# Kernel tuning notes

Measured on AMD Instinct MI355X. Metric: run time of the kernel, lower is better.

Reference implementation:

```python
import jax, jax.numpy as jnp
import numpy as np

N_USER, N_BADGE, E = 200_000, 50_000, 5_000_000
NEG_SLOPE = 0.2


def _gat(x_src, x_dst, src, dst, Ws, Wd, a_s, a_d, b, n_dst):
    """Bipartite single-head PyG GATConv (add_self_loops=False)."""
    hs = x_src @ Ws                      # [Ns, C]
    hd = x_dst @ Wd                      # [Nd, C]
    alpha_s = hs @ a_s                   # [Ns]
    alpha_d = hd @ a_d                   # [Nd]
    e = jax.nn.leaky_relu(alpha_s[src] + alpha_d[dst], NEG_SLOPE)  # [E]
    m = jax.ops.segment_max(e, dst, num_segments=n_dst)            # per-dst max
    w = jnp.exp(e - m[dst])
    s = jax.ops.segment_sum(w, dst, num_segments=n_dst) + 1e-16
    alpha = w / s[dst]                   # softmax over incoming edges
    out = jax.ops.segment_sum(alpha[:, None] * hs[src], dst, num_segments=n_dst)
    return out + b


def setup_inputs() -> dict:
    key = jax.random.key(0)
    ks = jax.random.split(key, 40)
    i = [0]
    def nk():
        k = ks[i[0]]; i[0] += 1; return k
    def nrm(shape, scale):
        return jax.random.normal(nk(), shape, jnp.float32) * scale
    inp = {
        "x_user": nrm((N_USER, 64), 1.0),
        "x_badge": nrm((N_BADGE, 64), 1.0),
        "ub_src": jax.random.randint(nk(), (E,), 0, N_USER, jnp.int32),
        "ub_dst": jax.random.randint(nk(), (E,), 0, N_BADGE, jnp.int32),
        "bu_src": jax.random.randint(nk(), (E,), 0, N_BADGE, jnp.int32),
        "bu_dst": jax.random.randint(nk(), (E,), 0, N_USER, jnp.int32),
        "ew_ub": jax.random.uniform(nk(), (E,), jnp.float32),
        "ew_bu": jax.random.uniform(nk(), (E,), jnp.float32),
    }
    s64, s16 = 1.0 / 8.0, 1.0 / 4.0  # ~glorot-ish scales for fan_in 64 / 16
    for rel in ("ub", "bu"):
        inp[f"W1_{rel}_s"] = nrm((64, 16), s64)
        inp[f"W1_{rel}_d"] = nrm((64, 16), s64)
        inp[f"a1_{rel}_s"] = nrm((16,), s16)
        inp[f"a1_{rel}_d"] = nrm((16,), s16)
        inp[f"b1_{rel}"] = jnp.zeros((16,), jnp.float32)
        inp[f"W2_{rel}_s"] = nrm((16, 2), s16)
        inp[f"W2_{rel}_d"] = nrm((16, 2), s16)
        inp[f"a2_{rel}_s"] = nrm((2,), 0.5)
        inp[f"a2_{rel}_d"] = nrm((2,), 0.5)
        inp[f"b2_{rel}"] = jnp.zeros((2,), jnp.float32)
    return inp


def reference(x_user, x_badge, ub_src, ub_dst, bu_src, bu_dst, ew_ub, ew_bu,
              W1_ub_s, W1_ub_d, a1_ub_s, a1_ub_d, b1_ub,
              W1_bu_s, W1_bu_d, a1_bu_s, a1_bu_d, b1_bu,
              W2_ub_s, W2_ub_d, a2_ub_s, a2_ub_d, b2_ub,
              W2_bu_s, W2_bu_d, a2_bu_s, a2_bu_d, b2_bu):
    # layer 1 (edge weights ignored: GATConv has edge_dim=None -> lin_edge is None)
    hb = _gat(x_user, x_badge, ub_src, ub_dst, W1_ub_s, W1_ub_d, a1_ub_s, a1_ub_d, b1_ub, N_BADGE)
    hu = _gat(x_badge, x_user, bu_src, bu_dst, W1_bu_s, W1_bu_d, a1_bu_s, a1_bu_d, b1_bu, N_USER)
    hu = jax.nn.relu(hu)
    hb = jax.nn.relu(hb)
    # layer 2
    ob = _gat(hu, hb, ub_src, ub_dst, W2_ub_s, W2_ub_d, a2_ub_s, a2_ub_d, b2_ub, N_BADGE)
    ou = _gat(hb, hu, bu_src, bu_dst, W2_bu_s, W2_bu_d, a2_bu_s, a2_bu_d, b2_bu, N_USER)
    return (ou, ob)
```

## Files before the change

### kernel.cpp

```cpp
#include <hip/hip_runtime.h>
#include <hip/hip_fp16.h>
#include <math.h>


#define NEG_SLOPE 0.2f
#define PART_PER 4880
#define NBC 196
#define CAPC 27072
#define NHALF 392
#define CAPH 13824
#define SHARD_DIV 50000

__device__ __forceinline__ float lrelu(float x) { return x > 0.f ? x : NEG_SLOPE * x; }

__global__ void k_stageA(
    const int* __restrict__ src0, const int* __restrict__ dst0,
    const int* __restrict__ src1, const int* __restrict__ dst1,
    int nE, int pblocks, unsigned* __restrict__ part0, unsigned* __restrict__ part1,
    int* __restrict__ bcnt,
    const float* __restrict__ xu, const float* __restrict__ xb,
    const float* __restrict__ Wub_s, const float* __restrict__ aub_s,
    const float* __restrict__ Wbu_d, const float* __restrict__ abu_d,
    const float* __restrict__ Wbu_s, const float* __restrict__ abu_s,
    const float* __restrict__ Wub_d, const float* __restrict__ aub_d,
    __half* __restrict__ hs_u, float* __restrict__ as_u, float* __restrict__ ad_u,
    __half* __restrict__ hs_b, float* __restrict__ as_b, float* __restrict__ ad_b,
    int NU, int NB, int gNU, int partBlocks, int nodeBlocks) {
  union Sm {
    struct { unsigned s_sorted[PART_PER]; int h[257]; int ps[256]; int resb[256]; int cur[256]; } p;
    struct { float sW[64 * 16]; float sa[16]; float sv[64]; } n;
  };
  __shared__ Sm sm;
  int t = threadIdx.x;
  int b = blockIdx.x;
  int k = min(nodeBlocks, partBlocks / 2);
  int inter = 3 * k;
  int partIdx = -1, nodeIdx = -1;
  if (b < inter) {
    if ((b % 3) == 2) nodeIdx = b / 3;
    else partIdx = (b / 3) * 2 + (b % 3);
  } else {
    int rem = b - inter;
    int ptail = partBlocks - 2 * k;
    if (rem < ptail) partIdx = 2 * k + rem;
    else nodeIdx = k + (rem - ptail);
  }
  if (partIdx >= 0) {
    int gb = partIdx;
    const int* src; const int* dst; unsigned* part; int* bc; int shift; int mask;
    if (gb < pblocks) { src = src0; dst = dst0; part = part0; bc = bcnt; shift = 8; mask = 255; }
    else { gb -= pblocks; src = src1; dst = dst1; part = part1; bc = bcnt + 256; shift = 10; mask = 1023; }
    int per = (nE + pblocks - 1) / pblocks;
    int beg = gb * per;
    int end = min(beg + per, nE);
    int cnt = end - beg;
    int cnt4 = cnt & ~3;
    sm.p.h[t] = 0;
    __syncthreads();
    for (int i = beg + t * 4; i + 3 < end; i += 1024) {
      int4 d4 = *(const int4*)(dst + i);
      atomicAdd(&sm.p.h[d4.x >> shift], 1);
      atomicAdd(&sm.p.h[d4.y >> shift], 1);
      atomicAdd(&sm.p.h[d4.z >> shift], 1);
      atomicAdd(&sm.p.h[d4.w >> shift], 1);
    }
    for (int i = beg + cnt4 + t; i < end; i += 256) atomicAdd(&sm.p.h[dst[i] >> shift], 1);
    __syncthreads();
    int v = sm.p.h[t];
    sm.p.ps[t] = v;
    __syncthreads();
    for (int off = 1; off < 256; off <<= 1) {
      int u = (t >= off) ? sm.p.ps[t - off] : 0;
      __syncthreads();
      sm.p.ps[t] += u;
      __syncthreads();
    }
    int excl = sm.p.ps[t] - v;
    sm.p.resb[t] = (t < NBC && v > 0) ? atomicAdd(&bc[t], v) : 0;
    __syncthreads();
    sm.p.h[t] = excl;
    sm.p.cur[t] = excl;
    if (t == 255) sm.p.h[256] = excl + v;
    __syncthreads();
    for (int i = beg + t * 4; i + 3 < end; i += 1024) {
      int4 d4 = *(const int4*)(dst + i);
      int4 s4 = *(const int4*)(src + i);
      int r;
      r = atomicAdd(&sm.p.cur[d4.x >> shift], 1);
      sm.p.s_sorted[r] = ((unsigned)(d4.x & mask) << 18) | (unsigned)s4.x;
      r = atomicAdd(&sm.p.cur[d4.y >> shift], 1);
      sm.p.s_sorted[r] = ((unsigned)(d4.y & mask) << 18) | (unsigned)s4.y;
      r = atomicAdd(&sm.p.cur[d4.z >> shift], 1);
      sm.p.s_sorted[r] = ((unsigned)(d4.z & mask) << 18) | (unsigned)s4.z;
      r = atomicAdd(&sm.p.cur[d4.w >> shift], 1);
      sm.p.s_sorted[r] = ((unsigned)(d4.w & mask) << 18) | (unsigned)s4.w;
    }
    for (int i = beg + cnt4 + t; i < end; i += 256) {
      int d = dst[i];
      int r = atomicAdd(&sm.p.cur[d >> shift], 1);
      sm.p.s_sorted[r] = ((unsigned)(d & mask) << 18) | (unsigned)src[i];
    }
    __syncthreads();
    for (int i = t; i < cnt; i += 1024) {
      int i1 = i + 256, i2 = i + 512, i3 = i + 768;
      int lo0 = 0, lo1 = 0, lo2 = 0, lo3 = 0;
      int hi0 = 256, hi1 = 256, hi2 = 256, hi3 = 256;
#pragma unroll
      for (int s = 0; s < 8; ++s) {
        int m0 = (lo0 + hi0) >> 1; if (sm.p.h[m0] <= i)  lo0 = m0; else hi0 = m0;
        int m1 = (lo1 + hi1) >> 1; if (sm.p.h[m1] <= i1) lo1 = m1; else hi1 = m1;
        int m2 = (lo2 + hi2) >> 1; if (sm.p.h[m2] <= i2) lo2 = m2; else hi2 = m2;
        int m3 = (lo3 + hi3) >> 1; if (sm.p.h[m3] <= i3) lo3 = m3; else hi3 = m3;
      }
      { int p = sm.p.resb[lo0] + (i - sm.p.h[lo0]);
        if (p < CAPC) part[(size_t)lo0 * CAPC + p] = sm.p.s_sorted[i]; }
      if (i1 < cnt) { int p = sm.p.resb[lo1] + (i1 - sm.p.h[lo1]);
        if (p < CAPC) part[(size_t)lo1 * CAPC + p] = sm.p.s_sorted[i1]; }
      if (i2 < cnt) { int p = sm.p.resb[lo2] + (i2 - sm.p.h[lo2]);
        if (p < CAPC) part[(size_t)lo2 * CAPC + p] = sm.p.s_sorted[i2]; }
      if (i3 < cnt) { int p = sm.p.resb[lo3] + (i3 - sm.p.h[lo3]);
        if (p < CAPC) part[(size_t)lo3 * CAPC + p] = sm.p.s_sorted[i3]; }
    }
    return;
  }
  int blk = nodeIdx;
  bool us = blk < gNU;
  const float* x  = us ? xu : xb;
  const float* Ws = us ? Wub_s : Wbu_s;
  const float* As = us ? aub_s : abu_s;
  const float* Wd = us ? Wbu_d : Wub_d;
  const float* Ad = us ? abu_d : aub_d;
  __half* hs = us ? hs_u : hs_b;
  float* als = us ? as_u : as_b;
  float* ald = us ? ad_u : ad_b;
  int N = us ? NU : NB;
  for (int i = t; i < 64 * 16; i += 256) sm.n.sW[i] = Ws[i];
  if (t < 16) sm.n.sa[t] = As[t];
  if (t < 64) {
    float s = 0.f;
    for (int c = 0; c < 16; ++c) s += Wd[t * 16 + c] * Ad[c];
    sm.n.sv[t] = s;
  }
  __syncthreads();
  int n = (us ? blk : blk - gNU) * 256 + t;
  if (n >= N) return;
  float acc[16];
#pragma unroll
  for (int c = 0; c < 16; ++c) acc[c] = 0.f;
  float ad = 0.f;
  const float4* xr4 = (const float4*)(x + (size_t)n * 64);
#pragma unroll 4
  for (int f4 = 0; f4 < 16; ++f4) {
    float4 xv4 = xr4[f4];
    float xv[4] = {xv4.x, xv4.y, xv4.z, xv4.w};
#pragma unroll
    for (int q = 0; q < 4; ++q) {
      int f = f4 * 4 + q;
#pragma unroll
      for (int c = 0; c < 16; ++c) acc[c] += xv[q] * sm.n.sW[f * 16 + c];
      ad += xv[q] * sm.n.sv[f];
    }
  }
  float al = 0.f;
#pragma unroll
  for (int c = 0; c < 16; ++c) {
    hs[(size_t)n * 16 + c] = __float2half(acc[c]);
    al += acc[c] * sm.n.sa[c];
  }
  als[n] = al;
  ald[n] = ad;
}

__global__ void k_sort2_both(const unsigned* __restrict__ part0,
                             const unsigned* __restrict__ part1,
                             const int* __restrict__ bcnt,
                             int* __restrict__ col0, int* __restrict__ col1,
                             int* __restrict__ rp0, int* __restrict__ rp1) {
  __shared__ unsigned s_sorted[CAPH];
  __shared__ int hist[512];
  __shared__ int ps[512];
  __shared__ int cur[512];
  __shared__ int s_tot;
  int bb = blockIdx.x;
  const unsigned* part; const int* bc; int* col; int* rp;
  int hsh, hmask, ns, sdiv;
  if (bb < NHALF) { part = part0; bc = bcnt; col = col0; rp = rp0;
                    hsh = 7; hmask = 127; ns = 4; sdiv = SHARD_DIV; }
  else { bb -= NHALF; part = part1; bc = bcnt + 256; col = col1; rp = rp1;
         hsh = 9; hmask = 511; ns = 1; sdiv = 1 << 30; }
  int t = threadIdx.x;
  int f = bb >> 1;
  int half = bb & 1;
  int cnt = min(bc[f], CAPC);
  int cnt4 = cnt & ~3;
  int slot = bb * CAPH;
  const unsigned* pp = part + (size_t)f * CAPC;
  hist[t] = 0;
  __syncthreads();
  for (int i = t * 4; i + 3 < cnt; i += 2048) {
    uint4 e4 = *(const uint4*)(pp + i);
    unsigned ee[4] = {e4.x, e4.y, e4.z, e4.w};
#pragma unroll
    for (int q = 0; q < 4; ++q) {
      int dl = (int)(ee[q] >> 18);
      if ((dl >> hsh) == half) {
        int sv = (int)(ee[q] & 0x3FFFFu);
        int bin = (ns == 4) ? ((dl & hmask) << 2) + sv / sdiv : (dl & hmask);
        atomicAdd(&hist[bin], 1);
      }
    }
  }
  for (int i = cnt4 + t; i < cnt; i += 512) {
    unsigned e = pp[i];
    int dl = (int)(e >> 18);
    if ((dl >> hsh) == half) {
      int sv = (int)(e & 0x3FFFFu);
      int bin = (ns == 4) ? ((dl & hmask) << 2) + sv / sdiv : (dl & hmask);
      atomicAdd(&hist[bin], 1);
    }
  }
  __syncthreads();
  int v = hist[t];
  ps[t] = v;
  __syncthreads();
  for (int off = 1; off < 512; off <<= 1) {
    int u = (t >= off) ? ps[t - off] : 0;
    __syncthreads();
    ps[t] += u;
    __syncthreads();
  }
  int excl = ps[t] - v;
  rp[bb * 513 + t] = slot + excl;
  if (t == 511) {
    int tot = min(ps[511], CAPH);
    rp[bb * 513 + 512] = slot + tot;
    s_tot = tot;
  }
  cur[t] = excl;
  __syncthreads();
  for (int i = t * 4; i + 3 < cnt; i += 2048) {
    uint4 e4 = *(const uint4*)(pp + i);
    unsigned ee[4] = {e4.x, e4.y, e4.z, e4.w};
#pragma unroll
    for (int q = 0; q < 4; ++q) {
      int dl = (int)(ee[q] >> 18);
      if ((dl >> hsh) == half) {
        int sv = (int)(ee[q] & 0x3FFFFu);
        int bin = (ns == 4) ? ((dl & hmask) << 2) + sv / sdiv : (dl & hmask);
        int r = atomicAdd(&cur[bin], 1);
        if (r < CAPH) s_sorted[r] = (unsigned)sv;
      }
    }
  }
  for (int i = cnt4 + t; i < cnt; i += 512) {
    unsigned e = pp[i];
    int dl = (int)(e >> 18);
    if ((dl >> hsh) == half) {
      int sv = (int)(e & 0x3FFFFu);
      int bin = (ns == 4) ? ((dl & hmask) << 2) + sv / sdiv : (dl & hmask);
      int r = atomicAdd(&cur[bin], 1);
      if (r < CAPH) s_sorted[r] = (unsigned)sv;
    }
  }
  __syncthreads();
  int tot = s_tot;
  for (int i = t; i < tot; i += 512) col[slot + i] = (int)s_sorted[i];
}

__device__ __forceinline__ void gat_pipe4(
    const int* __restrict__ col, const float* __restrict__ as,
    const __half* __restrict__ hs, int beg, int end, int j, float adv,
    float (&acc)[16], float& se) {
  int k0 = beg + j;
  if (k0 >= end) return;
  int sv0 = col[k0];
  int k1 = k0 + 4;
  int sv1 = (k1 < end) ? col[k1] : -1;
  float e0 = as[sv0];
  const uint4* hv0 = (const uint4*)(hs + (size_t)sv0 * 16);
  uint4 lo0 = hv0[0], hi0 = hv0[1];
  for (;;) {
    float e1 = 0.f;
    uint4 lo1 = lo0, hi1 = hi0;
    int sv2 = -1;
    int k2 = k1 + 4;
    if (sv1 >= 0) {
      e1 = as[sv1];
      const uint4* hv1 = (const uint4*)(hs + (size_t)sv1 * 16);
      lo1 = hv1[0];
      hi1 = hv1[1];
      sv2 = (k2 < end) ? col[k2] : -1;
    }
    float w = __expf(lrelu(e0 + adv));
    se += w;
    union { uint4 v[2]; __half h[16]; } b;
    b.v[0] = lo0;
    b.v[1] = hi0;
#pragma unroll
    for (int c = 0; c < 16; ++c) acc[c] += w * __half2float(b.h[c]);
    if (sv1 < 0) break;
    e0 = e1;
    lo0 = lo1;
    hi0 = hi1;
    sv1 = sv2;
    k1 = k2;
  }
}

__global__ void k_megaL1(
    const int* __restrict__ rp_ub, const int* __restrict__ col_ub,
    const float* __restrict__ as_u, const float* __restrict__ ad_b,
    const __half* __restrict__ hs_u,
    float* __restrict__ acc_sl, float* __restrict__ se_sl,
    const int* __restrict__ rp_bu, const int* __restrict__ col_bu,
    const float* __restrict__ as_b, const float* __restrict__ ad_u,
    const __half* __restrict__ hs_b,
    const float* __restrict__ b1bu,
    const float* __restrict__ W2ub_s, const float* __restrict__ a2ub_s,
    const float* __restrict__ W2bu_d, const float* __restrict__ a2bu_d,
    float4* __restrict__ pk_u, int NB, int NU, int ubBlocks) {
  __shared__ float sW2[32], sa2[2], sv2[16], sb1[16];
  int t = threadIdx.x;
  if (t < 32) sW2[t] = W2ub_s[t];
  if (t < 2) sa2[t] = a2ub_s[t];
  if (t < 16) {
    float s = 0.f;
    for (int cc = 0; cc < 2; ++cc) s += W2bu_d[t * 2 + cc] * a2bu_d[cc];
    sv2[t] = s;
    sb1[t] = b1bu[t];
  }
  __syncthreads();
  int b = blockIdx.x;
  int j = t & 3;
  if (b < ubBlocks) {
    int xcd = b & 7;
    int s = xcd >> 1;
    int sub = ((b >> 3) << 1) | (xcd & 1);
    int n = sub * 64 + (t >> 2);
    if (n >= NB) return;
    int base = (n >> 7) * 513 + (n & 127) * 4 + s;
    int beg = rp_ub[base], end = rp_ub[base + 1];
    float adv = ad_b[n];
    float acc[16];
#pragma unroll
    for (int c = 0; c < 16; ++c) acc[c] = 0.f;
    float se = 0.f;
    gat_pipe4(col_ub, as_u, hs_u, beg, end, j, adv, acc, se);
#pragma unroll
    for (int m = 1; m < 4; m <<= 1) {
      se += __shfl_xor(se, m, 4);
#pragma unroll
      for (int c = 0; c < 16; ++c) acc[c] += __shfl_xor(acc[c], m, 4);
    }
    if (j == 0) {
      float* o = acc_sl + ((size_t)s * NB + n) * 16;
#pragma unroll
      for (int c = 0; c < 16; ++c) o[c] = acc[c];
      se_sl[s * NB + n] = se;
    }
  } else {
    int n = (b - ubBlocks) * 64 + (t >> 2);
    if (n >= NU) return;
    int base = (n >> 9) * 513 + (n & 511);
    int beg = rp_bu[base], end = rp_bu[base + 1];
    float adv = ad_u[n];
    float acc[16];
#pragma unroll
    for (int c = 0; c < 16; ++c) acc[c] = 0.f;
    float se = 0.f;
    gat_pipe4(col_bu, as_b, hs_b, beg, end, j, adv, acc, se);
#pragma unroll
    for (int m = 1; m < 4; m <<= 1) {
      se += __shfl_xor(se, m, 4);
#pragma unroll
      for (int c = 0; c < 16; ++c) acc[c] += __shfl_xor(acc[c], m, 4);
    }
    if (j == 0) {
      float inv = 1.f / (se + 1e-16f);
      float h0 = 0.f, h1 = 0.f, advn = 0.f;
#pragma unroll
      for (int c = 0; c < 16; ++c) {
        float xv = fmaxf(acc[c] * inv + sb1[c], 0.f);
        h0 += xv * sW2[c * 2];
        h1 += xv * sW2[c * 2 + 1];
        advn += xv * sv2[c];
      }
      pk_u[n] = make_float4(h0 * sa2[0] + h1 * sa2[1], h0, h1, advn);
    }
  }
}

__global__ void k_finL1b(
    const float* __restrict__ acc_sl, const float* __restrict__ se_sl,
    const float* __restrict__ b1ub,
    const float* __restrict__ W2bu_s, const float* __restrict__ a2bu_s,
    const float* __restrict__ W2ub_d, const float* __restrict__ a2ub_d,
    float4* __restrict__ pk_b, int NB) {
  __shared__ float sW2[32], sa2[2], sv2[16], sb1[16];
  int t = threadIdx.x;
  if (t < 32) sW2[t] = W2bu_s[t];
  if (t < 2) sa2[t] = a2bu_s[t];
  if (t < 16) {
    float s = 0.f;
    for (int cc = 0; cc < 2; ++cc) s += W2ub_d[t * 2 + cc] * a2ub_d[cc];
    sv2[t] = s;
    sb1[t] = b1ub[t];
  }
  __syncthreads();
  int n = blockIdx.x * 256 + t;
  if (n >= NB) return;
  float a[16];
#pragma unroll
  for (int c = 0; c < 16; ++c) a[c] = 0.f;
  float se = 0.f;
  for (int s = 0; s < 4; ++s) {
    const float4* p = (const float4*)(acc_sl + ((size_t)s * NB + n) * 16);
    float4 v0 = p[0], v1 = p[1], v2 = p[2], v3 = p[3];
    a[0] += v0.x; a[1] += v0.y; a[2] += v0.z; a[3] += v0.w;
    a[4] += v1.x; a[5] += v1.y; a[6] += v1.z; a[7] += v1.w;
    a[8] += v2.x; a[9] += v2.y; a[10] += v2.z; a[11] += v2.w;
    a[12] += v3.x; a[13] += v3.y; a[14] += v3.z; a[15] += v3.w;
    se += se_sl[s * NB + n];
  }
  float inv = 1.f / (se + 1e-16f);
  float h0 = 0.f, h1 = 0.f, advn = 0.f;
#pragma unroll
  for (int c = 0; c < 16; ++c) {
    float xv = fmaxf(a[c] * inv + sb1[c], 0.f);
    h0 += xv * sW2[c * 2];
    h1 += xv * sW2[c * 2 + 1];
    advn += xv * sv2[c];
  }
  pk_b[n] = make_float4(h0 * sa2[0] + h1 * sa2[1], h0, h1, advn);
}

__global__ void k_gatherL2(
    const int* __restrict__ rp0, const int* __restrict__ col0,
    const int* __restrict__ rp1, const int* __restrict__ col1,
    const float4* __restrict__ pk_u, const float4* __restrict__ pk_b,
    const float* __restrict__ b2ub, const float* __restrict__ b2bu,
    float* __restrict__ ob, float* __restrict__ ou,
    int NB, int NU, int g0) {
  int blk = blockIdx.x;
  const int *rp, *col; const float4 *pksrc, *pkown; const float* bb; float* out;
  int N, lsh, nsg;
  if (blk < g0) { rp = rp0; col = col0; pksrc = pk_u; pkown = pk_b; bb = b2ub;
                  out = ob; N = NB; lsh = 7; nsg = 4; }
  else { blk -= g0; rp = rp1; col = col1; pksrc = pk_b; pkown = pk_u; bb = b2bu;
         out = ou; N = NU; lsh = 9; nsg = 1; }
  int n = blk * 64 + (threadIdx.x >> 2);
  int j = threadIdx.x & 3;
  if (n >= N) return;
  int base = (n >> lsh) * 513 + (n & ((1 << lsh) - 1)) * nsg;
  int beg = rp[base], end = rp[base + nsg];
  float adv = pkown[n].w;
  float a0 = 0.f, a1 = 0.f, se = 0.f;
  int k0 = beg + j;
  if (k0 < end) {
    int c0 = col[k0];
    int k1 = k0 + 4;
    int c1 = (k1 < end) ? col[k1] : -1;
    float4 p0 = pksrc[c0];
    for (;;) {
      float4 p1 = p0;
      int c2 = -1;
      int k2 = k1 + 4;
      if (c1 >= 0) {
        p1 = pksrc[c1];
        c2 = (k2 < end) ? col[k2] : -1;
      }
      float w = __expf(lrelu(p0.x + adv));
      se += w;
      a0 += w * p0.y;
      a1 += w * p0.z;
      if (c1 < 0) break;
      p0 = p1;
      c1 = c2;
      k1 = k2;
    }
  }
#pragma unroll
  for (int m = 1; m < 4; m <<= 1) {
    se += __shfl_xor(se, m, 4);
    a0 += __shfl_xor(a0, m, 4);
    a1 += __shfl_xor(a1, m, 4);
  }
  if (j == 0) {
    float inv = 1.f / (se + 1e-16f);
    out[(size_t)n * 2] = a0 * inv + bb[0];
    out[(size_t)n * 2 + 1] = a1 * inv + bb[1];
  }
}

extern "C" void kernel_launch(void* const* d_in, const int* in_sizes, int n_in,
                              void* d_out, int out_size, void* d_ws, size_t ws_size,
                              hipStream_t stream) {
  const int NU = 200000, NB = 50000;
  const float* x_user  = (const float*)d_in[0];
  const float* x_badge = (const float*)d_in[1];
  const int* ub_src = (const int*)d_in[2];
  const int* ub_dst = (const int*)d_in[3];
  const int* bu_src = (const int*)d_in[4];
  const int* bu_dst = (const int*)d_in[5];
  const int nE = in_sizes[2];

  const float* W1_ub_s = (const float*)d_in[8];
  const float* W1_ub_d = (const float*)d_in[9];
  const float* a1_ub_s = (const float*)d_in[10];
  const float* a1_ub_d = (const float*)d_in[11];
  const float* b1_ub   = (const float*)d_in[12];
  const float* W2_ub_s = (const float*)d_in[13];
  const float* W2_ub_d = (const float*)d_in[14];
  const float* a2_ub_s = (const float*)d_in[15];
  const float* a2_ub_d = (const float*)d_in[16];
  const float* b2_ub   = (const float*)d_in[17];
  const float* W1_bu_s = (const float*)d_in[18];
  const float* W1_bu_d = (const float*)d_in[19];
  const float* a1_bu_s = (const float*)d_in[20];
  const float* a1_bu_d = (const float*)d_in[21];
  const float* b1_bu   = (const float*)d_in[22];
  const float* W2_bu_s = (const float*)d_in[23];
  const float* W2_bu_d = (const float*)d_in[24];
  const float* a2_bu_s = (const float*)d_in[25];
  const float* a2_bu_d = (const float*)d_in[26];
  const float* b2_bu   = (const float*)d_in[27];

  const int pblocks = (nE + PART_PER - 1) / PART_PER;
  const int gNU = (NU + 255) / 256;
  const int gNB = (NB + 255) / 256;

  char* wsb = (char*)d_ws;
  size_t off = 0;
  auto ialloc = [&](size_t n) { int* p = (int*)(wsb + off); off += n * 4; return p; };
  int* rp2_ub = ialloc((size_t)NHALF * 513);
  int* rp2_bu = ialloc((size_t)NHALF * 513);
  int* bcnt   = ialloc(512);
  int* col_ub = ialloc((size_t)NHALF * CAPH);
  int* col_bu = ialloc((size_t)NHALF * CAPH);
  off = (off + 15) & ~(size_t)15;
  const size_t partBytes = (size_t)2 * NBC * CAPC * 4;
  const size_t nodeBytes = (size_t)NU * 32 + (size_t)NB * 32 +
                           (size_t)(NU + NB) * 8 + 1024;
  bool fused = ws_size >= off + partBytes + nodeBytes + 4096;
  char* partBase = wsb + off;
  char* nodeBase = fused ? (partBase + partBytes) : partBase;
  unsigned* part0 = (unsigned*)partBase;
  unsigned* part1 = part0 + (size_t)NBC * CAPC;
  size_t poff = 0;
  auto falloc = [&](size_t n) { float* p = (float*)(nodeBase + poff); poff += n * 4; return p; };
  auto halloc = [&](size_t n) { __half* p = (__half*)(nodeBase + poff); poff += n * 2; return p; };
  __half* hs_u1 = halloc((size_t)NU * 16);
  __half* hs_b1 = halloc((size_t)NB * 16);
  float* as_u1  = falloc(NU);
  float* ad_u1  = falloc(NU);
  float* as_b1  = falloc(NB);
  float* ad_b1  = falloc(NB);
  poff = (poff + 15) & ~(size_t)15;
  float4* pk_u  = (float4*)(nodeBase + poff); poff += (size_t)NU * 16;
  float4* pk_b  = (float4*)(nodeBase + poff); poff += (size_t)NB * 16;
  char* accBase = fused ? partBase : (nodeBase + ((poff + 15) & ~(size_t)15));
  float* acc_sl = (float*)accBase;
  float* se_sl  = (float*)(accBase + (size_t)4 * NB * 16 * 4);

  float* ou = (float*)d_out;
  float* ob = (float*)d_out + (size_t)NU * 2;

  const int chunksB = (NB + 63) / 64;
  const int ubBlocks = ((chunksB + 1) / 2) * 8;
  const int buBlocks = (NU + 63) / 64;
  const int g0 = (NB + 63) / 64;

  hipMemsetAsync(bcnt, 0, 512 * 4, stream);
  if (fused) {
    k_stageA<<<dim3(2 * pblocks + gNU + gNB), dim3(256), 0, stream>>>(
        ub_src, ub_dst, bu_src, bu_dst, nE, pblocks, part0, part1, bcnt,
        x_user, x_badge, W1_ub_s, a1_ub_s, W1_bu_d, a1_bu_d,
        W1_bu_s, a1_bu_s, W1_ub_d, a1_ub_d,
        hs_u1, as_u1, ad_u1, hs_b1, as_b1, ad_b1, NU, NB, gNU,
        2 * pblocks, gNU + gNB);
    k_sort2_both<<<dim3(2 * NHALF), dim3(512), 0, stream>>>(
        part0, part1, bcnt, col_ub, col_bu, rp2_ub, rp2_bu);
  } else {
    k_stageA<<<dim3(2 * pblocks), dim3(256), 0, stream>>>(
        ub_src, ub_dst, bu_src, bu_dst, nE, pblocks, part0, part1, bcnt,
        x_user, x_badge, W1_ub_s, a1_ub_s, W1_bu_d, a1_bu_d,
        W1_bu_s, a1_bu_s, W1_ub_d, a1_ub_d,
        hs_u1, as_u1, ad_u1, hs_b1, as_b1, ad_b1, NU, NB, gNU,
        2 * pblocks, 0);
    k_sort2_both<<<dim3(2 * NHALF), dim3(512), 0, stream>>>(
        part0, part1, bcnt, col_ub, col_bu, rp2_ub, rp2_bu);
    k_stageA<<<dim3(gNU + gNB), dim3(256), 0, stream>>>(
        ub_src, ub_dst, bu_src, bu_dst, nE, pblocks, part0, part1, bcnt,
        x_user, x_badge, W1_ub_s, a1_ub_s, W1_bu_d, a1_bu_d,
        W1_bu_s, a1_bu_s, W1_ub_d, a1_ub_d,
        hs_u1, as_u1, ad_u1, hs_b1, as_b1, ad_b1, NU, NB, gNU,
        0, gNU + gNB);
  }
  k_megaL1<<<dim3(ubBlocks + buBlocks), dim3(256), 0, stream>>>(
      rp2_ub, col_ub, as_u1, ad_b1, hs_u1, acc_sl, se_sl,
      rp2_bu, col_bu, as_b1, ad_u1, hs_b1,
      b1_bu, W2_ub_s, a2_ub_s, W2_bu_d, a2_bu_d,
      pk_u, NB, NU, ubBlocks);
  k_finL1b<<<dim3(gNB), dim3(256), 0, stream>>>(
      acc_sl, se_sl, b1_ub, W2_bu_s, a2_bu_s, W2_ub_d, a2_ub_d, pk_b, NB);
  k_gatherL2<<<dim3(g0 + buBlocks), dim3(256), 0, stream>>>(
      rp2_ub, col_ub, rp2_bu, col_bu, pk_u, pk_b, b2_ub, b2_bu, ob, ou, NB, NU, g0);
}
```

Measured before the change: 470.6 us.

## Split layer-1 GAT rows across lane pairs and recompute source attention from features

The layer-1 aggregation now uses 8 lanes per destination node, with pairs of lanes each loading one 8-channel half of the fp16 source feature row. The separate per-source attention-logit gather is dropped: the logit is recomputed as a dot product of the half-precision features with a1_s, combined across the lane pair with a shuffle. This removes one random 4-byte gather per edge and doubles thread-level parallelism, but halves nodes per block, adds shuffles, and computes the logit from fp16-rounded features, which may change accuracy slightly.

```diff
diff --git a/kernel.cpp b/kernel.cpp
--- a/kernel.cpp
+++ b/kernel.cpp
@@ -267,41 +267,41 @@
   for (int i = t; i < tot; i += 512) col[slot + i] = (int)s_sorted[i];
 }
 
-__device__ __forceinline__ void gat_pipe4(
-    const int* __restrict__ col, const float* __restrict__ as,
-    const __half* __restrict__ hs, int beg, int end, int j, float adv,
-    float (&acc)[16], float& se) {
-  int k0 = beg + j;
+__device__ __forceinline__ void gat_pair8(
+    const int* __restrict__ col, const __half* __restrict__ hs,
+    int beg, int end, int j, float adv, const float (&sa)[8],
+    float (&acc)[8], float& se) {
+  int h = j & 1;
+  int k0 = beg + (j >> 1);
   if (k0 >= end) return;
   int sv0 = col[k0];
   int k1 = k0 + 4;
   int sv1 = (k1 < end) ? col[k1] : -1;
-  float e0 = as[sv0];
-  const uint4* hv0 = (const uint4*)(hs + (size_t)sv0 * 16);
-  uint4 lo0 = hv0[0], hi0 = hv0[1];
+  uint4 hv0 = *(const uint4*)(hs + (size_t)sv0 * 16 + h * 8);
   for (;;) {
-    float e1 = 0.f;
-    uint4 lo1 = lo0, hi1 = hi0;
+    uint4 hv1 = hv0;
     int sv2 = -1;
     int k2 = k1 + 4;
     if (sv1 >= 0) {
-      e1 = as[sv1];
-      const uint4* hv1 = (const uint4*)(hs + (size_t)sv1 * 16);
-      lo1 = hv1[0];
-      hi1 = hv1[1];
+      hv1 = *(const uint4*)(hs + (size_t)sv1 * 16 + h * 8);
       sv2 = (k2 < end) ? col[k2] : -1;
     }
-    float w = __expf(lrelu(e0 + adv));
+    union { uint4 v; __half hh[8]; } b;
+    b.v = hv0;
+    float f[8];
+    float p = 0.f;
+#pragma unroll
+    for (int cc = 0; cc < 8; ++cc) {
+      f[cc] = __half2float(b.hh[cc]);
+      p += f[cc] * sa[cc];
+    }
+    float afull = p + __shfl_xor(p, 1, 8);
+    float w = __expf(lrelu(afull + adv));
     se += w;
-    union { uint4 v[2]; __half h[16]; } b;
-    b.v[0] = lo0;
-    b.v[1] = hi0;
-#pragma unroll
-    for (int c = 0; c < 16; ++c) acc[c] += w * __half2float(b.h[c]);
+#pragma unroll
+    for (int cc = 0; cc < 8; ++cc) acc[cc] += w * f[cc];
     if (sv1 < 0) break;
-    e0 = e1;
-    lo0 = lo1;
-    hi0 = hi1;
+    hv0 = hv1;
     sv1 = sv2;
     k1 = k2;
   }
@@ -309,17 +309,17 @@
 
 __global__ void k_megaL1(
     const int* __restrict__ rp_ub, const int* __restrict__ col_ub,
-    const float* __restrict__ as_u, const float* __restrict__ ad_b,
+    const float* __restrict__ a1s_ub, const float* __restrict__ ad_b,
     const __half* __restrict__ hs_u,
     float* __restrict__ acc_sl, float* __restrict__ se_sl,
     const int* __restrict__ rp_bu, const int* __restrict__ col_bu,
-    const float* __restrict__ as_b, const float* __restrict__ ad_u,
+    const float* __restrict__ a1s_bu, const float* __restrict__ ad_u,
     const __half* __restrict__ hs_b,
     const float* __restrict__ b1bu,
     const float* __restrict__ W2ub_s, const float* __restrict__ a2ub_s,
     const float* __restrict__ W2bu_d, const float* __restrict__ a2bu_d,
     float4* __restrict__ pk_u, int NB, int NU, int ubBlocks) {
-  __shared__ float sW2[32], sa2[2], sv2[16], sb1[16];
+  __shared__ float sW2[32], sa2[2], sv2[16], sb1[16], sAub[16], sAbu[16];
   int t = threadIdx.x;
   if (t < 32) sW2[t] = W2ub_s[t];
   if (t < 2) sa2[t] = a2ub_s[t];
@@ -328,65 +328,77 @@
     for (int cc = 0; cc < 2; ++cc) s += W2bu_d[t * 2 + cc] * a2bu_d[cc];
     sv2[t] = s;
     sb1[t] = b1bu[t];
+    sAub[t] = a1s_ub[t];
+    sAbu[t] = a1s_bu[t];
   }
   __syncthreads();
   int b = blockIdx.x;
-  int j = t & 3;
+  int j = t & 7;
+  int h = j & 1;
   if (b < ubBlocks) {
     int xcd = b & 7;
     int s = xcd >> 1;
     int sub = ((b >> 3) << 1) | (xcd & 1);
-    int n = sub * 64 + (t >> 2);
+    int n = sub * 32 + (t >> 3);
     if (n >= NB) return;
     int base = (n >> 7) * 513 + (n & 127) * 4 + s;
     int beg = rp_ub[base], end = rp_ub[base + 1];
     float adv = ad_b[n];
-    float acc[16];
-#pragma unroll
-    for (int c = 0; c < 16; ++c) acc[c] = 0.f;
+    float sa[8];
+#pragma unroll
+    for (int cc = 0; cc < 8; ++cc) sa[cc] = sAub[h * 8 + cc];
+    float acc[8];
+#pragma unroll
+    for (int cc = 0; cc < 8; ++cc) acc[cc] = 0.f;
     float se = 0.f;
-    gat_pipe4(col_ub, as_u, hs_u, beg, end, j, adv, acc, se);
-#pragma unroll
-    for (int m = 1; m < 4; m <<= 1) {
-      se += __shfl_xor(se, m, 4);
-#pragma unroll
-      for (int c = 0; c < 16; ++c) acc[c] += __shfl_xor(acc[c], m, 4);
-    }
-    if (j == 0) {
-      float* o = acc_sl + ((size_t)s * NB + n) * 16;
-#pragma unroll
-      for (int c = 0; c < 16; ++c) o[c] = acc[c];
-      se_sl[s * NB + n] = se;
+    gat_pair8(col_ub, hs_u, beg, end, j, adv, sa, acc, se);
+#pragma unroll
+    for (int m = 2; m < 8; m <<= 1) {
+      se += __shfl_xor(se, m, 8);
+#pragma unroll
+      for (int cc = 0; cc < 8; ++cc) acc[cc] += __shfl_xor(acc[cc], m, 8);
+    }
+    if (j < 2) {
+      float* o = acc_sl + ((size_t)s * NB + n) * 16 + h * 8;
+#pragma unroll
+      for (int cc = 0; cc < 8; ++cc) o[cc] = acc[cc];
+      if (j == 0) se_sl[s * NB + n] = se;
     }
   } else {
-    int n = (b - ubBlocks) * 64 + (t >> 2);
+    int n = (b - ubBlocks) * 32 + (t >> 3);
     if (n >= NU) return;
     int base = (n >> 9) * 513 + (n & 511);
     int beg = rp_bu[base], end = rp_bu[base + 1];
     float adv = ad_u[n];
-    float acc[16];
-#pragma unroll
-    for (int c = 0; c < 16; ++c) acc[c] = 0.f;
+    float sa[8];
+#pragma unroll
+    for (int cc = 0; cc < 8; ++cc) sa[cc] = sAbu[h * 8 + cc];
+    float acc[8];
+#pragma unroll
+    for (int cc = 0; cc < 8; ++cc) acc[cc] = 0.f;
     float se = 0.f;
-    gat_pipe4(col_bu, as_b, hs_b, beg, end, j, adv, acc, se);
-#pragma unroll
-    for (int m = 1; m < 4; m <<= 1) {
-      se += __shfl_xor(se, m, 4);
-#pragma unroll
-      for (int c = 0; c < 16; ++c) acc[c] += __shfl_xor(acc[c], m, 4);
-    }
-    if (j == 0) {
-      float inv = 1.f / (se + 1e-16f);
-      float h0 = 0.f, h1 = 0.f, advn = 0.f;
-#pragma unroll
-      for (int c = 0; c < 16; ++c) {
-        float xv = fmaxf(acc[c] * inv + sb1[c], 0.f);
-        h0 += xv * sW2[c * 2];
-        h1 += xv * sW2[c * 2 + 1];
-        advn += xv * sv2[c];
-      }
-      pk_u[n] = make_float4(h0 * sa2[0] + h1 * sa2[1], h0, h1, advn);
-    }
+    gat_pair8(col_bu, hs_b, beg, end, j, adv, sa, acc, se);
+#pragma unroll
+    for (int m = 2; m < 8; m <<= 1) {
+      se += __shfl_xor(se, m, 8);
+#pragma unroll
+      for (int cc = 0; cc < 8; ++cc) acc[cc] += __shfl_xor(acc[cc], m, 8);
+    }
+    float inv = 1.f / (se + 1e-16f);
+    float ph0 = 0.f, ph1 = 0.f, padv = 0.f;
+#pragma unroll
+    for (int cc = 0; cc < 8; ++cc) {
+      int c = h * 8 + cc;
+      float xv = fmaxf(acc[cc] * inv + sb1[c], 0.f);
+      ph0 += xv * sW2[c * 2];
+      ph1 += xv * sW2[c * 2 + 1];
+      padv += xv * sv2[c];
+    }
+    ph0 += __shfl_xor(ph0, 1, 8);
+    ph1 += __shfl_xor(ph1, 1, 8);
+    padv += __shfl_xor(padv, 1, 8);
+    if (j == 0)
+      pk_u[n] = make_float4(ph0 * sa2[0] + ph1 * sa2[1], ph0, ph1, padv);
   }
 }
 
@@ -565,10 +577,11 @@
   float* ou = (float*)d_out;
   float* ob = (float*)d_out + (size_t)NU * 2;
 
-  const int chunksB = (NB + 63) / 64;
+  const int chunksB = (NB + 31) / 32;
   const int ubBlocks = ((chunksB + 1) / 2) * 8;
-  const int buBlocks = (NU + 63) / 64;
+  const int buBlocks = (NU + 31) / 32;
   const int g0 = (NB + 63) / 64;
+  const int g1 = (NU + 63) / 64;
 
   hipMemsetAsync(bcnt, 0, 512 * 4, stream);
   if (fused) {
@@ -597,12 +610,12 @@
         0, gNU + gNB);
   }
   k_megaL1<<<dim3(ubBlocks + buBlocks), dim3(256), 0, stream>>>(
-      rp2_ub, col_ub, as_u1, ad_b1, hs_u1, acc_sl, se_sl,
-      rp2_bu, col_bu, as_b1, ad_u1, hs_b1,
+      rp2_ub, col_ub, a1_ub_s, ad_b1, hs_u1, acc_sl, se_sl,
+      rp2_bu, col_bu, a1_bu_s, ad_u1, hs_b1,
       b1_bu, W2_ub_s, a2_ub_s, W2_bu_d, a2_bu_d,
       pk_u, NB, NU, ubBlocks);
   k_finL1b<<<dim3(gNB), dim3(256), 0, stream>>>(
       acc_sl, se_sl, b1_ub, W2_bu_s, a2_bu_s, W2_ub_d, a2_ub_d, pk_b, NB);
-  k_gatherL2<<<dim3(g0 + buBlocks), dim3(256), 0, stream>>>(
+  k_gatherL2<<<dim3(g0 + g1), dim3(256), 0, stream>>>(
       rp2_ub, col_ub, rp2_bu, col_bu, pk_u, pk_b, b2_ub, b2_bu, ob, ou, NB, NU, g0);
 }
```

Result: faster. 430.3 us (-8.6%).
